# Kernel tuning notes

Measured on AMD Instinct MI355X. Metric: run time of the kernel, lower is better.

## Reference

```python
import jax, jax.numpy as jnp
import numpy as np

PS = 8          # patch_size
NF = 16         # n_feats
B, H, W = 4, 256, 256
C = NF * PS * PS          # channel_num = 1024
INNER = 3 * C             # heads * channel_num (no head split in source)
SCALE = C ** -0.5         # heads_feats = channel_num
EPS = 1e-5


def _patch(x, shift):
    # reflect-pad then non-overlapping unfold (kernel=PS, stride=PS)
    s = PS // 4
    p = shift * s
    x = jnp.pad(x, ((0, 0), (0, 0), (p, PS - p), (p, PS - p)), mode='reflect')
    b, c, hp, wp = x.shape
    x = x.reshape(b, c, hp // PS, PS, wp // PS, PS)
    # F.unfold ordering: (c, kh, kw) flattened per patch, patches row-major
    x = x.transpose(0, 2, 4, 1, 3, 5).reshape(b, (hp // PS) * (wp // PS), c * PS * PS)
    return x  # [B, N, C*PS*PS]


def _unpatch(x, h, w):
    # inverse of non-overlapping unfold, then crop right/bottom by PS
    b, n, d = x.shape
    c = d // (PS * PS)
    nh, nw = (h + PS) // PS, (w + PS) // PS
    x = x.reshape(b, nh, nw, c, PS, PS).transpose(0, 3, 1, 4, 2, 5)
    x = x.reshape(b, c, nh * PS, nw * PS)
    return x[:, :, :h, :w]


def _ln(x, g, b):
    m = x.mean(-1, keepdims=True)
    v = ((x - m) ** 2).mean(-1, keepdims=True)
    return (x - m) / jnp.sqrt(v + EPS) * g + b


def setup_inputs():
    key = jax.random.key(0)
    ks = jax.random.split(key, 16)
    w = lambda k, shp: jax.random.normal(k, shp, jnp.float32) * 0.02
    return {
        'dr_img': jax.random.normal(ks[0], (B, NF, H, W), jnp.float32),
        'dr_ref': jax.random.normal(ks[1], (B, NF, H, W), jnp.float32),
        'cl_ref': jax.random.normal(ks[2], (B, NF, H, W), jnp.float32),
        'ln_g': jnp.ones((C,), jnp.float32), 'ln_b': jnp.zeros((C,), jnp.float32),
        'Wq': w(ks[3], (C, INNER)), 'bq': jnp.zeros((INNER,), jnp.float32),
        'Wk': w(ks[4], (C, INNER)), 'bk': jnp.zeros((INNER,), jnp.float32),
        'Wv': w(ks[5], (C, INNER)), 'bv': jnp.zeros((INNER,), jnp.float32),
        'Wo': w(ks[6], (INNER, C)), 'bo': jnp.zeros((C,), jnp.float32),
        'ff_ln_g': jnp.ones((C,), jnp.float32), 'ff_ln_b': jnp.zeros((C,), jnp.float32),
        'W1': w(ks[7], (C, C)), 'b1': jnp.zeros((C,), jnp.float32),
        'W2': w(ks[8], (C, C)), 'b2': jnp.zeros((C,), jnp.float32),
    }


def reference(dr_img, dr_ref, cl_ref, ln_g, ln_b, Wq, bq, Wk, bk, Wv, bv,
              Wo, bo, ff_ln_g, ff_ln_b, W1, b1, W2, b2):
    def attn(q, k, v):
        qp = _ln(q, ln_g, ln_b) @ Wq + bq          # [B,N,3C]
        kp = _ln(k, ln_g, ln_b) @ Wk + bk
        vp = _ln(v, ln_g, ln_b) @ Wv + bv
        a = jax.nn.softmax(jnp.einsum('bnd,bmd->bnm', qp, kp) * SCALE, axis=-1)
        return jnp.einsum('bnm,bmd->bnd', a, vp) @ Wo + bo

    def ff(x):
        h = _ln(x, ff_ln_g, ff_ln_b)
        return jax.nn.gelu(h @ W1 + b1, approximate=False) @ W2 + b2

    x = _patch(dr_img, 0)                           # [B,N,C]
    for shift in range(4):
        k = jax.lax.stop_gradient(_patch(dr_ref, shift))
        v = jax.lax.stop_gradient(_patch(cl_ref, shift))
        x = attn(x, k, v) + x
        x = ff(x) + x
    return _unpatch(x, H, W)
```

## Files before the change

kernel.cpp:

```cpp
#include <hip/hip_runtime.h>

typedef unsigned short u16;
typedef float f32x4 __attribute__((ext_vector_type(4)));
typedef __bf16 bf16v8 __attribute__((ext_vector_type(8)));
typedef u16 u16x4 __attribute__((ext_vector_type(4)));

#define WAITV(n) asm volatile("s_waitcnt vmcnt(" #n ")" ::: "memory")
#define BAR() asm volatile("s_barrier" ::: "memory")
#define LGKM0() do { asm volatile("s_waitcnt lgkmcnt(0)" ::: "memory"); \
                     __builtin_amdgcn_sched_barrier(0); } while (0)

__device__ __forceinline__ u16 f2bf(float f) {
  union { float f; unsigned int u; } v; v.f = f;
  unsigned int x = v.u;
  x += 0x7fffu + ((x >> 16) & 1u);
  return (u16)(x >> 16);
}

__device__ __forceinline__ int refl(int i, int n) {
  i = (i < 0) ? -i : i;
  return (i >= n) ? (2 * n - 2 - i) : i;
}

__device__ __forceinline__ void gload_lds16(const void* g, void* l) {
  __builtin_amdgcn_global_load_lds(
      (const __attribute__((address_space(1))) void*)g,
      (__attribute__((address_space(3))) void*)l, 16, 0, 0);
}

enum { EPI_BF16_BIAS = 0, EPI_F32 = 1, EPI_BF16 = 2, EPI_F32_RES = 3, EPI_GELU = 4 };

__device__ __forceinline__ void xcd_remap(int& bx, int& by, int& bz) {
  const int gx = gridDim.x, gy = gridDim.y;
  const int nwg = gx * gy * (int)gridDim.z;
  const int orig = ((int)blockIdx.z * gy + (int)blockIdx.y) * gx + (int)blockIdx.x;
  const int q = nwg >> 3, r = nwg & 7;
  const int xcd = orig & 7, loc = orig >> 3;
  const int swz = (xcd < r ? xcd * (q + 1) : r * (q + 1) + (xcd - r) * q) + loc;
  const int gxy = gx * gy;
  bz = swz / gxy;
  const int rem = swz - bz * gxy;
  by = rem / gx; bx = rem - by * gx;
}

template <int EPI>
__global__ __launch_bounds__(512, 2) void gemm256(
    const u16* __restrict__ A, const u16* __restrict__ Bt, void* __restrict__ Cp,
    const float* __restrict__ bias, int K, int Nld, long sA, long sB, long sC, long sBias)
{
  extern __shared__ __align__(16) u16 smem[];

  const int t = threadIdx.x;
  int bx, by, bz; xcd_remap(bx, by, bz);
  const int m0 = by * 256, n0 = bx * 256;

  const long Kb = (long)K * 2;
  const int sr8 = t >> 3;
  const int schunk = ((t & 7) ^ (sr8 & 7)) * 16;
  const char* Ag = (const char*)(A + (long)bz * sA + (long)m0 * K) + (long)sr8 * Kb + schunk;
  const char* Bg = (const char*)(Bt + (long)bz * sB + (long)n0 * K) + (long)sr8 * Kb + schunk;

  auto SA = [&](int d, int kt, int i0, int i1) {
    const long ko = (long)kt * 128;
    gload_lds16(Ag + (long)i0 * 64 * Kb + ko, &smem[d * 32768 + i0 * 4096 + t * 8]);
    gload_lds16(Ag + (long)i1 * 64 * Kb + ko, &smem[d * 32768 + i1 * 4096 + t * 8]);
  };
  auto SB = [&](int d, int kt, int i0, int i1) {
    const long ko = (long)kt * 128;
    gload_lds16(Bg + (long)i0 * 64 * Kb + ko, &smem[d * 32768 + 16384 + i0 * 4096 + t * 8]);
    gload_lds16(Bg + (long)i1 * 64 * Kb + ko, &smem[d * 32768 + 16384 + i1 * 4096 + t * 8]);
  };

  const int w = t >> 6, lane = t & 63;
  const int wm = (w >> 2) * 128, wn = (w & 3) * 64;
  const int lr = lane & 15, hi = lane >> 4;
  const int rc0 = ((0 * 4 + hi) ^ (lr & 7)) * 8;
  const int rc1 = ((1 * 4 + hi) ^ (lr & 7)) * 8;

  f32x4 acc[8][4];
  const f32x4 vzero = {0.f, 0.f, 0.f, 0.f};
#pragma unroll
  for (int i = 0; i < 8; i++)
#pragma unroll
    for (int j = 0; j < 4; j++) acc[i][j] = vzero;

  const int NT = K >> 6, NI = NT >> 1;

  SA(0, 0, 0, 1); SA(0, 0, 2, 3); SB(0, 0, 0, 1); SB(0, 0, 2, 3);
  SB(1, 1, 0, 2); SB(1, 1, 1, 3); SA(1, 1, 0, 2);
  WAITV(6);
  BAR();

  for (int i = 0; i < NI; i++) {
    const int t0 = 2 * i;
    const bool last = (i == NI - 1);
#pragma unroll
    for (int h = 0; h < 2; h++) {
      const u16* Ad = &smem[h * 32768];
      const u16* Bd = Ad + 16384;
      bf16v8 b8[4][2];
#pragma unroll
      for (int q = 0; q < 4; q++) {
        bf16v8 a8[2][2];
#pragma unroll
        for (int j = 0; j < 2; j++) {
          const int rbase = (wm + (2 * q + j) * 16 + lr) * 64;
          a8[j][0] = *(const bf16v8*)&Ad[rbase + rc0];
          a8[j][1] = *(const bf16v8*)&Ad[rbase + rc1];
        }
        if (q == 0) {
#pragma unroll
          for (int ni = 0; ni < 4; ni++) {
            const int rbase = (wn + ni * 16 + lr) * 64;
            b8[ni][0] = *(const bf16v8*)&Bd[rbase + rc0];
            b8[ni][1] = *(const bf16v8*)&Bd[rbase + rc1];
          }
        }
        if (h == 0) {
          if (q == 0)           SA(1, t0 + 1, 1, 3);
          else if (!last) {
            if (q == 1)         SB(0, t0 + 2, 0, 2);
            else if (q == 2)    SB(0, t0 + 2, 1, 3);
            else                SA(0, t0 + 2, 0, 2);
          }
        } else if (!last) {
          if (q == 0)           SA(0, t0 + 2, 1, 3);
          else if (q == 1)      SB(1, t0 + 3, 0, 2);
          else if (q == 2)      SB(1, t0 + 3, 1, 3);
          else                  SA(1, t0 + 3, 0, 2);
        }
        BAR();
        LGKM0();
        __builtin_amdgcn_s_setprio(1);
#pragma unroll
        for (int j = 0; j < 2; j++)
#pragma unroll
          for (int ni = 0; ni < 4; ni++) {
            acc[2 * q + j][ni] = __builtin_amdgcn_mfma_f32_16x16x32_bf16(a8[j][0], b8[ni][0], acc[2 * q + j][ni], 0, 0, 0);
            acc[2 * q + j][ni] = __builtin_amdgcn_mfma_f32_16x16x32_bf16(a8[j][1], b8[ni][1], acc[2 * q + j][ni], 0, 0, 0);
          }
        __builtin_amdgcn_s_setprio(0);
        if (h == 0 && q == 3) { if (last) { WAITV(0); } else { WAITV(6); } }
        if (h == 1 && q == 3 && !last) { WAITV(6); }
        BAR();
      }
    }
  }

#pragma unroll
  for (int mi = 0; mi < 8; mi++) {
    const int r0 = m0 + wm + mi * 16 + hi * 4;
#pragma unroll
    for (int ni = 0; ni < 4; ni++) {
      const int col = n0 + wn + ni * 16 + lr;
      float bvv = 0.f;
      if constexpr (EPI == EPI_BF16_BIAS) bvv = bias[bz * sBias + col];
#pragma unroll
      for (int j = 0; j < 4; j++) {
        const long idx = (long)(r0 + j) * Nld + col;
        const float val = acc[mi][ni][j] + bvv;
        if constexpr (EPI == EPI_BF16_BIAS || EPI == EPI_BF16) {
          ((u16*)Cp + (long)bz * sC)[idx] = f2bf(val);
        } else {
          ((float*)Cp + (long)bz * sC)[idx] = val;
        }
      }
    }
  }
}

template <int EPI>
__global__ __launch_bounds__(256, 2) void gemm128(
    const u16* __restrict__ A, const u16* __restrict__ Bt, void* __restrict__ Cp,
    const float* __restrict__ bias, int K, int Nld, long sA, long sB, long sC)
{
  extern __shared__ __align__(16) u16 smem[];
  u16* As = smem;
  u16* Bs = smem + 16384;

  const int t = threadIdx.x;
  int bx, by, bz; xcd_remap(bx, by, bz);
  const int m0 = by * 128, n0 = bx * 128;

  const long Kb = (long)K * 2;
  const int sc = ((t & 7) * 16) ^ (((t >> 3) & 7) << 4);
  const char* Ag = (const char*)(A + (long)bz * sA + (long)m0 * K) + (long)(t >> 3) * Kb + sc;
  const char* Bg = (const char*)(Bt + (long)bz * sB + (long)n0 * K) + (long)(t >> 3) * Kb + sc;

  auto STAGE = [&](int d, int kt) {
    const long ko = (long)kt * 128;
#pragma unroll
    for (int i = 0; i < 4; i++)
      gload_lds16(Ag + (long)i * 32 * Kb + ko, &As[d * 8192 + i * 2048 + t * 8]);
#pragma unroll
    for (int i = 0; i < 4; i++)
      gload_lds16(Bg + (long)i * 32 * Kb + ko, &Bs[d * 8192 + i * 2048 + t * 8]);
  };

  const int w = t >> 6, lane = t & 63;
  const int wm = (w >> 1) * 64, wn = (w & 1) * 64;
  const int lr = lane & 15, hi = lane >> 4;
  const int cx = (lr & 7) << 4;

  f32x4 acc[4][4];
  const f32x4 vzero = {0.f, 0.f, 0.f, 0.f};
#pragma unroll
  for (int i = 0; i < 4; i++)
#pragma unroll
    for (int j = 0; j < 4; j++) acc[i][j] = vzero;

  const int NT = K >> 6;
  STAGE(0, 0);
  STAGE(1, 1);

  for (int kt = 0; kt < NT; kt++) {
    const int d = kt & 1;
    if (kt + 1 < NT) { WAITV(8); } else { WAITV(0); }
    BAR();

    const u16* Ad = &As[d * 8192];
    const u16* Bd = &Bs[d * 8192];
#pragma unroll
    for (int ks = 0; ks < 2; ks++) {
      bf16v8 a8[4], b8[4];
      const int cb = ks * 64;
#pragma unroll
      for (int mi = 0; mi < 4; mi++)
        a8[mi] = *(const bf16v8*)&Ad[(wm + mi * 16 + lr) * 64 + (((cb + hi * 16) ^ cx) >> 1)];
#pragma unroll
      for (int ni = 0; ni < 4; ni++)
        b8[ni] = *(const bf16v8*)&Bd[(wn + ni * 16 + lr) * 64 + (((cb + hi * 16) ^ cx) >> 1)];
      __builtin_amdgcn_s_setprio(1);
#pragma unroll
      for (int mi = 0; mi < 4; mi++)
#pragma unroll
        for (int ni = 0; ni < 4; ni++)
          acc[mi][ni] = __builtin_amdgcn_mfma_f32_16x16x32_bf16(a8[mi], b8[ni], acc[mi][ni], 0, 0, 0);
      __builtin_amdgcn_s_setprio(0);
    }
    asm volatile("s_waitcnt lgkmcnt(0)\n\ts_barrier" ::: "memory");
    if (kt + 2 < NT) STAGE(d, kt + 2);
  }

#pragma unroll
  for (int mi = 0; mi < 4; mi++) {
    const int r0 = m0 + wm + mi * 16 + hi * 4;
#pragma unroll
    for (int ni = 0; ni < 4; ni++) {
      const int col = n0 + wn + ni * 16 + lr;
      float bvv = 0.f;
      if constexpr (EPI == EPI_F32_RES || EPI == EPI_GELU) bvv = bias[col];
#pragma unroll
      for (int j = 0; j < 4; j++) {
        const long idx = (long)(r0 + j) * Nld + col;
        const float val = acc[mi][ni][j] + bvv;
        if constexpr (EPI == EPI_F32) {
          ((float*)Cp + (long)bz * sC)[idx] = val;
        } else if constexpr (EPI == EPI_F32_RES) {
          ((float*)Cp)[idx] += val;
        } else if constexpr (EPI == EPI_GELU) {
          const float gv = 0.5f * val * (1.f + erff(val * 0.70710678118654752440f));
          ((u16*)Cp)[idx] = f2bf(gv);
        } else {
          ((u16*)Cp)[idx] = f2bf(val);
        }
      }
    }
  }
}

__global__ __launch_bounds__(256) void ln_kernel(const float* __restrict__ X,
    const float* __restrict__ g, const float* __restrict__ be, u16* __restrict__ Y)
{
  const long row = blockIdx.x;
  const int t = threadIdx.x;
  const float* xr = X + row * 1024;
  f32x4 v = *(const f32x4*)&xr[t * 4];
  float s = v[0] + v[1] + v[2] + v[3];
  float q = v[0]*v[0] + v[1]*v[1] + v[2]*v[2] + v[3]*v[3];
#pragma unroll
  for (int off = 32; off; off >>= 1) { s += __shfl_xor(s, off); q += __shfl_xor(q, off); }
  __shared__ float red[8];
  if ((t & 63) == 0) { red[t >> 6] = s; red[4 + (t >> 6)] = q; }
  __syncthreads();
  s = red[0] + red[1] + red[2] + red[3];
  q = red[4] + red[5] + red[6] + red[7];
  const float mean = s * (1.f / 1024.f);
  const float rstd = rsqrtf(q * (1.f / 1024.f) - mean * mean + 1e-5f);
  f32x4 gv = *(const f32x4*)&g[t * 4];
  f32x4 bv = *(const f32x4*)&be[t * 4];
  u16x4 o;
#pragma unroll
  for (int i = 0; i < 4; i++) o[i] = f2bf((v[i] - mean) * rstd * gv[i] + bv[i]);
  *(u16x4*)&Y[row * 1024 + t * 4] = o;
}

__global__ __launch_bounds__(256) void patch_kernel(const float* __restrict__ img,
    float* __restrict__ X, int shift)
{
  const int n = blockIdx.x, b = blockIdx.y, t = threadIdx.x;
  float* xr = X + ((long)b * 1280 + n) * 1024;
  if (n >= 1089) {
    const f32x4 z = {0.f, 0.f, 0.f, 0.f};
    *(f32x4*)&xr[t * 4] = z;
    return;
  }
  const int p = shift * 2;
  const int ph = n / 33, pw = n - ph * 33;
  const int d0 = t * 4;
  const int c = d0 >> 6, kh = (d0 >> 3) & 7, kw0 = d0 & 7;
  const int hh = refl(ph * 8 + kh - p, 256);
  const float* src = img + ((long)(b * 16 + c) * 256 + hh) * 256;
  f32x4 v;
#pragma unroll
  for (int i = 0; i < 4; i++) v[i] = src[refl(pw * 8 + kw0 + i - p, 256)];
  *(f32x4*)&xr[d0] = v;
}

__global__ __launch_bounds__(256) void patch_ln_kernel(const float* __restrict__ img,
    const float* __restrict__ g, const float* __restrict__ be, u16* __restrict__ Y, int shift)
{
  const int n = blockIdx.x, b = blockIdx.y, t = threadIdx.x;
  u16* yr = Y + ((long)b * 1280 + n) * 1024;
  if (n >= 1089) {
    const u16x4 z = {0, 0, 0, 0};
    *(u16x4*)&yr[t * 4] = z;
    return;
  }
  const int p = shift * 2;
  const int ph = n / 33, pw = n - ph * 33;
  const int d0 = t * 4;
  const int c = d0 >> 6, kh = (d0 >> 3) & 7, kw0 = d0 & 7;
  const int hh = refl(ph * 8 + kh - p, 256);
  const float* src = img + ((long)(b * 16 + c) * 256 + hh) * 256;
  float v[4];
#pragma unroll
  for (int i = 0; i < 4; i++) v[i] = src[refl(pw * 8 + kw0 + i - p, 256)];
  float s = v[0] + v[1] + v[2] + v[3];
  float q = v[0]*v[0] + v[1]*v[1] + v[2]*v[2] + v[3]*v[3];
#pragma unroll
  for (int off = 32; off; off >>= 1) { s += __shfl_xor(s, off); q += __shfl_xor(q, off); }
  __shared__ float red[8];
  if ((t & 63) == 0) { red[t >> 6] = s; red[4 + (t >> 6)] = q; }
  __syncthreads();
  s = red[0] + red[1] + red[2] + red[3];
  q = red[4] + red[5] + red[6] + red[7];
  const float mean = s * (1.f / 1024.f);
  const float rstd = rsqrtf(q * (1.f / 1024.f) - mean * mean + 1e-5f);
  u16x4 o;
#pragma unroll
  for (int i = 0; i < 4; i++) o[i] = f2bf((v[i] - mean) * rstd * g[d0 + i] + be[d0 + i]);
  *(u16x4*)&yr[d0] = o;
}

__global__ __launch_bounds__(256) void softmax_kernel(const float* __restrict__ L,
    u16* __restrict__ P)
{
  const int r = blockIdx.x, b = blockIdx.y, t = threadIdx.x;
  const float* Lr = L + ((long)b * 1280 + r) * 1280;
  u16* Pr = P + ((long)b * 1280 + r) * 1280;
  float v[5];
  float mx = -1e30f;
#pragma unroll
  for (int i = 0; i < 5; i++) {
    const int j = t + i * 256;
    v[i] = (j < 1089) ? Lr[j] * 0.03125f : -1e30f;
    mx = fmaxf(mx, v[i]);
  }
#pragma unroll
  for (int off = 32; off; off >>= 1) mx = fmaxf(mx, __shfl_xor(mx, off));
  __shared__ float sm[4];
  if ((t & 63) == 0) sm[t >> 6] = mx;
  __syncthreads();
  mx = fmaxf(fmaxf(sm[0], sm[1]), fmaxf(sm[2], sm[3]));
  float p[5];
  float s = 0.f;
#pragma unroll
  for (int i = 0; i < 5; i++) {
    const int j = t + i * 256;
    p[i] = (j < 1089) ? __expf(v[i] - mx) : 0.f;
    s += p[i];
  }
#pragma unroll
  for (int off = 32; off; off >>= 1) s += __shfl_xor(s, off);
  __shared__ float ss[4];
  if ((t & 63) == 0) ss[t >> 6] = s;
  __syncthreads();
  const float inv = 1.f / (ss[0] + ss[1] + ss[2] + ss[3]);
#pragma unroll
  for (int i = 0; i < 5; i++) Pr[t + i * 256] = f2bf(p[i] * inv);
}

__global__ __launch_bounds__(256) void vtrans_kernel(const u16* __restrict__ V,
    u16* __restrict__ Vt)
{
  __shared__ u16 tile[32][33];
  const int b = blockIdx.z;
  const int d0 = blockIdx.x * 32, m0 = blockIdx.y * 32;
  const int tx = threadIdx.x & 31, ty = threadIdx.x >> 5;
  const u16* Vb = V + (long)b * 1280 * 3072;
  u16* Vtb = Vt + (long)b * 3072 * 1280;
#pragma unroll
  for (int i = 0; i < 4; i++)
    tile[ty + 8 * i][tx] = Vb[(long)(m0 + ty + 8 * i) * 3072 + d0 + tx];
  __syncthreads();
#pragma unroll
  for (int i = 0; i < 4; i++)
    Vtb[(long)(d0 + ty + 8 * i) * 1280 + m0 + tx] = tile[tx][ty + 8 * i];
}

__global__ __launch_bounds__(256) void wtrans_kernel(const float* __restrict__ W,
    u16* __restrict__ Wt, int K, int N)
{
  __shared__ float tile[32][33];
  const int n0 = blockIdx.x * 32, k0 = blockIdx.y * 32;
  const int tx = threadIdx.x & 31, ty = threadIdx.x >> 5;
#pragma unroll
  for (int i = 0; i < 4; i++)
    tile[ty + 8 * i][tx] = W[(long)(k0 + ty + 8 * i) * N + n0 + tx];
  __syncthreads();
#pragma unroll
  for (int i = 0; i < 4; i++)
    Wt[(long)(n0 + ty + 8 * i) * K + k0 + tx] = f2bf(tile[tx][ty + 8 * i]);
}

__global__ __launch_bounds__(256) void catbias_kernel(const float* __restrict__ a,
    const float* __restrict__ b, const float* __restrict__ c, float* __restrict__ o)
{
  const int i = blockIdx.x * 256 + threadIdx.x;
  o[i] = a[i]; o[3072 + i] = b[i]; o[6144 + i] = c[i];
}

__global__ __launch_bounds__(256) void unpatch_kernel(const float* __restrict__ X,
    float* __restrict__ out)
{
  const int idx = blockIdx.x * 256 + threadIdx.x;
  const int w = (idx & 63) * 4;
  const int h = (idx >> 6) & 255;
  const int c = (idx >> 14) & 15;
  const int b = idx >> 18;
  const int ph = h >> 3, kh = h & 7, pw = w >> 3, kw = w & 7;
  const long row = (long)b * 1280 + ph * 33 + pw;
  const int d = c * 64 + kh * 8 + kw;
  const f32x4 v = *(const f32x4*)&X[row * 1024 + d];
  *(f32x4*)&out[((long)(b * 16 + c) * 256 + h) * 256 + w] = v;
}

extern "C" void kernel_launch(void* const* d_in, const int* in_sizes, int n_in,
                              void* d_out, int out_size, void* d_ws, size_t ws_size,
                              hipStream_t stream)
{
  (void)in_sizes; (void)n_in; (void)out_size; (void)ws_size;
  const float* dr_img = (const float*)d_in[0];
  const float* dr_ref = (const float*)d_in[1];
  const float* cl_ref = (const float*)d_in[2];
  const float* ln_g = (const float*)d_in[3];
  const float* ln_be = (const float*)d_in[4];
  const float* Wq = (const float*)d_in[5];
  const float* bq = (const float*)d_in[6];
  const float* Wk = (const float*)d_in[7];
  const float* bk = (const float*)d_in[8];
  const float* Wv = (const float*)d_in[9];
  const float* bv = (const float*)d_in[10];
  const float* Wo = (const float*)d_in[11];
  const float* bo = (const float*)d_in[12];
  const float* ffg = (const float*)d_in[13];
  const float* ffb = (const float*)d_in[14];
  const float* W1 = (const float*)d_in[15];
  const float* b1 = (const float*)d_in[16];
  const float* W2 = (const float*)d_in[17];
  const float* b2 = (const float*)d_in[18];

  const long R = 1280;
  const long MR = 4 * R;

  char* ws = (char*)d_ws;
  size_t off = 0;
  auto alloc = [&](size_t bytes) -> void* {
    void* pp = ws + off;
    off += (bytes + 255) & ~(size_t)255;
    return pp;
  };
  float* x    = (float*)alloc((size_t)MR * 1024 * 4);
  u16* xkv_ln = (u16*)alloc((size_t)3 * MR * 1024 * 2);
  u16* qkv    = (u16*)alloc((size_t)3 * MR * 3072 * 2);
  float* lgt  = (float*)alloc((size_t)4 * R * R * 4);
  u16* P      = (u16*)alloc((size_t)4 * R * R * 2);
  u16* Wqkv_t = (u16*)alloc((size_t)3 * 3072 * 1024 * 2);
  u16* Wo_t   = (u16*)alloc((size_t)1024 * 3072 * 2);
  u16* W1_t   = (u16*)alloc((size_t)1024 * 1024 * 2);
  u16* W2_t   = (u16*)alloc((size_t)1024 * 1024 * 2);
  float* bcat = (float*)alloc((size_t)3 * 3072 * 4);

  u16* x_ln = xkv_ln;
  u16* h    = xkv_ln + (size_t)MR * 1024;
  u16* qp   = qkv;
  u16* kp   = qkv + (size_t)MR * 3072;
  u16* vp   = qkv + (size_t)2 * MR * 3072;

  wtrans_kernel<<<dim3(96, 32), 256, 0, stream>>>(Wq, Wqkv_t, 1024, 3072);
  wtrans_kernel<<<dim3(96, 32), 256, 0, stream>>>(Wk, Wqkv_t + (size_t)3072 * 1024, 1024, 3072);
  wtrans_kernel<<<dim3(96, 32), 256, 0, stream>>>(Wv, Wqkv_t + (size_t)2 * 3072 * 1024, 1024, 3072);
  wtrans_kernel<<<dim3(32, 96), 256, 0, stream>>>(Wo, Wo_t, 3072, 1024);
  wtrans_kernel<<<dim3(32, 32), 256, 0, stream>>>(W1, W1_t, 1024, 1024);
  wtrans_kernel<<<dim3(32, 32), 256, 0, stream>>>(W2, W2_t, 1024, 1024);
  catbias_kernel<<<12, 256, 0, stream>>>(bq, bk, bv, bcat);

  patch_kernel<<<dim3(1280, 4), 256, 0, stream>>>(dr_img, x, 0);

  const long sAp = (long)MR * 1024;
  const long sBp = (long)3072 * 1024;
  const long sCp = (long)MR * 3072;
  const long sQb = R * 3072;
  const long sLb = R * R;

  for (int shift = 0; shift < 4; shift++) {
    ln_kernel<<<(int)MR, 256, 0, stream>>>(x, ln_g, ln_be, x_ln);
    patch_ln_kernel<<<dim3(1280, 4), 256, 0, stream>>>(dr_ref, ln_g, ln_be, xkv_ln + sAp, shift);
    patch_ln_kernel<<<dim3(1280, 4), 256, 0, stream>>>(cl_ref, ln_g, ln_be, xkv_ln + 2 * sAp, shift);

    gemm256<EPI_BF16_BIAS><<<dim3(12, 20, 3), 512, 131072, stream>>>(
        xkv_ln, Wqkv_t, qkv, bcat, 1024, 3072, sAp, sBp, sCp, 3072);

    gemm128<EPI_F32><<<dim3(10, 10, 4), 256, 65536, stream>>>(
        qp, kp, lgt, nullptr, 3072, 1280, sQb, sQb, sLb);

    softmax_kernel<<<dim3(1280, 4), 256, 0, stream>>>(lgt, P);
    vtrans_kernel<<<dim3(96, 40, 4), 256, 0, stream>>>(vp, kp);

    gemm256<EPI_BF16><<<dim3(12, 5, 4), 512, 131072, stream>>>(
        P, kp, qp, nullptr, 1280, 3072, sLb, (long)3072 * R, sQb, 0);

    gemm128<EPI_F32_RES><<<dim3(8, 40, 1), 256, 65536, stream>>>(
        qp, Wo_t, x, bo, 3072, 1024, 0, 0, 0);

    ln_kernel<<<(int)MR, 256, 0, stream>>>(x, ffg, ffb, x_ln);
    gemm128<EPI_GELU><<<dim3(8, 40, 1), 256, 65536, stream>>>(
        x_ln, W1_t, h, b1, 1024, 1024, 0, 0, 0);
    gemm128<EPI_F32_RES><<<dim3(8, 40, 1), 256, 65536, stream>>>(
        h, W2_t, x, b2, 1024, 1024, 0, 0, 0);
  }

  unpatch_kernel<<<4096, 256, 0, stream>>>(x, (float*)d_out);
}
```

Baseline: 1.486 ms.

## Shrink per-batch padding to 1152 rows and compute V projection pre-transposed

Per-batch patch rows are now padded to 1152 instead of 1280, which trims wasted rows from every GEMM, softmax and LN launch; the attention GEMMs, which scale quadratically with row count, shrink the most. The V projection becomes its own GEMM computing Wv^T·LN(v)^T with a per-row bias epilogue, so V comes out already transposed. That removes the separate vtrans kernel. The PV product moves to the 128-tile GEMM, which gains a separate B leading dimension and batch stride on its outputs. The risks are correctness of the padded-key handling at the new size and a worse tile fit for the split V GEMM.

After: 1.408 ms. 5.3% less time.

```diff
diff --git a/kernel.cpp b/kernel.cpp
--- a/kernel.cpp
+++ b/kernel.cpp
@@ -28,7 +28,8 @@
       (__attribute__((address_space(3))) void*)l, 16, 0, 0);
 }
 
-enum { EPI_BF16_BIAS = 0, EPI_F32 = 1, EPI_BF16 = 2, EPI_F32_RES = 3, EPI_GELU = 4 };
+enum { EPI_BF16_BIAS = 0, EPI_F32 = 1, EPI_BF16 = 2, EPI_F32_RES = 3, EPI_GELU = 4,
+       EPI_BF16_BIASROW = 5 };
 
 __device__ __forceinline__ void xcd_remap(int& bx, int& by, int& bz) {
   const int gx = gridDim.x, gy = gridDim.y;
@@ -158,8 +159,9 @@
 #pragma unroll
       for (int j = 0; j < 4; j++) {
         const long idx = (long)(r0 + j) * Nld + col;
-        const float val = acc[mi][ni][j] + bvv;
-        if constexpr (EPI == EPI_BF16_BIAS || EPI == EPI_BF16) {
+        float val = acc[mi][ni][j] + bvv;
+        if constexpr (EPI == EPI_BF16_BIASROW) val += bias[r0 + j];
+        if constexpr (EPI == EPI_BF16_BIAS || EPI == EPI_BF16 || EPI == EPI_BF16_BIASROW) {
           ((u16*)Cp + (long)bz * sC)[idx] = f2bf(val);
         } else {
           ((float*)Cp + (long)bz * sC)[idx] = val;
@@ -172,7 +174,7 @@
 template <int EPI>
 __global__ __launch_bounds__(256, 2) void gemm128(
     const u16* __restrict__ A, const u16* __restrict__ Bt, void* __restrict__ Cp,
-    const float* __restrict__ bias, int K, int Nld, long sA, long sB, long sC)
+    const float* __restrict__ bias, int K, int ldb, int Nld, long sA, long sB, long sC)
 {
   extern __shared__ __align__(16) u16 smem[];
   u16* As = smem;
@@ -182,19 +184,20 @@
   int bx, by, bz; xcd_remap(bx, by, bz);
   const int m0 = by * 128, n0 = bx * 128;
 
-  const long Kb = (long)K * 2;
+  const long Ka = (long)K * 2;
+  const long Kbb = (long)ldb * 2;
   const int sc = ((t & 7) * 16) ^ (((t >> 3) & 7) << 4);
-  const char* Ag = (const char*)(A + (long)bz * sA + (long)m0 * K) + (long)(t >> 3) * Kb + sc;
-  const char* Bg = (const char*)(Bt + (long)bz * sB + (long)n0 * K) + (long)(t >> 3) * Kb + sc;
+  const char* Ag = (const char*)(A + (long)bz * sA + (long)m0 * K) + (long)(t >> 3) * Ka + sc;
+  const char* Bg = (const char*)(Bt + (long)bz * sB + (long)n0 * ldb) + (long)(t >> 3) * Kbb + sc;
 
   auto STAGE = [&](int d, int kt) {
     const long ko = (long)kt * 128;
 #pragma unroll
     for (int i = 0; i < 4; i++)
-      gload_lds16(Ag + (long)i * 32 * Kb + ko, &As[d * 8192 + i * 2048 + t * 8]);
+      gload_lds16(Ag + (long)i * 32 * Ka + ko, &As[d * 8192 + i * 2048 + t * 8]);
 #pragma unroll
     for (int i = 0; i < 4; i++)
-      gload_lds16(Bg + (long)i * 32 * Kb + ko, &Bs[d * 8192 + i * 2048 + t * 8]);
+      gload_lds16(Bg + (long)i * 32 * Kbb + ko, &Bs[d * 8192 + i * 2048 + t * 8]);
   };
 
   const int w = t >> 6, lane = t & 63;
@@ -257,12 +260,12 @@
         if constexpr (EPI == EPI_F32) {
           ((float*)Cp + (long)bz * sC)[idx] = val;
         } else if constexpr (EPI == EPI_F32_RES) {
-          ((float*)Cp)[idx] += val;
+          ((float*)Cp + (long)bz * sC)[idx] += val;
         } else if constexpr (EPI == EPI_GELU) {
           const float gv = 0.5f * val * (1.f + erff(val * 0.70710678118654752440f));
-          ((u16*)Cp)[idx] = f2bf(gv);
+          ((u16*)Cp + (long)bz * sC)[idx] = f2bf(gv);
         } else {
-          ((u16*)Cp)[idx] = f2bf(val);
+          ((u16*)Cp + (long)bz * sC)[idx] = f2bf(val);
         }
       }
     }
@@ -299,7 +302,7 @@
     float* __restrict__ X, int shift)
 {
   const int n = blockIdx.x, b = blockIdx.y, t = threadIdx.x;
-  float* xr = X + ((long)b * 1280 + n) * 1024;
+  float* xr = X + ((long)b * 1152 + n) * 1024;
   if (n >= 1089) {
     const f32x4 z = {0.f, 0.f, 0.f, 0.f};
     *(f32x4*)&xr[t * 4] = z;
@@ -321,7 +324,7 @@
     const float* __restrict__ g, const float* __restrict__ be, u16* __restrict__ Y, int shift)
 {
   const int n = blockIdx.x, b = blockIdx.y, t = threadIdx.x;
-  u16* yr = Y + ((long)b * 1280 + n) * 1024;
+  u16* yr = Y + ((long)b * 1152 + n) * 1024;
   if (n >= 1089) {
     const u16x4 z = {0, 0, 0, 0};
     *(u16x4*)&yr[t * 4] = z;
@@ -357,8 +360,8 @@
     u16* __restrict__ P)
 {
   const int r = blockIdx.x, b = blockIdx.y, t = threadIdx.x;
-  const float* Lr = L + ((long)b * 1280 + r) * 1280;
-  u16* Pr = P + ((long)b * 1280 + r) * 1280;
+  const float* Lr = L + ((long)b * 1152 + r) * 1152;
+  u16* Pr = P + ((long)b * 1152 + r) * 1152;
   float v[5];
   float mx = -1e30f;
 #pragma unroll
@@ -388,25 +391,10 @@
   __syncthreads();
   const float inv = 1.f / (ss[0] + ss[1] + ss[2] + ss[3]);
 #pragma unroll
-  for (int i = 0; i < 5; i++) Pr[t + i * 256] = f2bf(p[i] * inv);
-}
-
-__global__ __launch_bounds__(256) void vtrans_kernel(const u16* __restrict__ V,
-    u16* __restrict__ Vt)
-{
-  __shared__ u16 tile[32][33];
-  const int b = blockIdx.z;
-  const int d0 = blockIdx.x * 32, m0 = blockIdx.y * 32;
-  const int tx = threadIdx.x & 31, ty = threadIdx.x >> 5;
-  const u16* Vb = V + (long)b * 1280 * 3072;
-  u16* Vtb = Vt + (long)b * 3072 * 1280;
-#pragma unroll
-  for (int i = 0; i < 4; i++)
-    tile[ty + 8 * i][tx] = Vb[(long)(m0 + ty + 8 * i) * 3072 + d0 + tx];
-  __syncthreads();
-#pragma unroll
-  for (int i = 0; i < 4; i++)
-    Vtb[(long)(d0 + ty + 8 * i) * 1280 + m0 + tx] = tile[tx][ty + 8 * i];
+  for (int i = 0; i < 5; i++) {
+    const int j = t + i * 256;
+    if (j < 1152) Pr[j] = f2bf(p[i] * inv);
+  }
 }
 
 __global__ __launch_bounds__(256) void wtrans_kernel(const float* __restrict__ W,
@@ -440,7 +428,7 @@
   const int c = (idx >> 14) & 15;
   const int b = idx >> 18;
   const int ph = h >> 3, kh = h & 7, pw = w >> 3, kw = w & 7;
-  const long row = (long)b * 1280 + ph * 33 + pw;
+  const long row = (long)b * 1152 + ph * 33 + pw;
   const int d = c * 64 + kh * 8 + kw;
   const f32x4 v = *(const f32x4*)&X[row * 1024 + d];
   *(f32x4*)&out[((long)(b * 16 + c) * 256 + h) * 256 + w] = v;
@@ -471,7 +459,7 @@
   const float* W2 = (const float*)d_in[17];
   const float* b2 = (const float*)d_in[18];
 
-  const long R = 1280;
+  const long R = 1152;
   const long MR = 4 * R;
 
   char* ws = (char*)d_ws;
@@ -493,20 +481,22 @@
   float* bcat = (float*)alloc((size_t)3 * 3072 * 4);
 
   u16* x_ln = xkv_ln;
+  u16* v_ln = xkv_ln + (size_t)2 * MR * 1024;
   u16* h    = xkv_ln + (size_t)MR * 1024;
   u16* qp   = qkv;
   u16* kp   = qkv + (size_t)MR * 3072;
-  u16* vp   = qkv + (size_t)2 * MR * 3072;
+  u16* vT   = qkv + (size_t)2 * MR * 3072;
+  u16* Wv_t = Wqkv_t + (size_t)2 * 3072 * 1024;
 
   wtrans_kernel<<<dim3(96, 32), 256, 0, stream>>>(Wq, Wqkv_t, 1024, 3072);
   wtrans_kernel<<<dim3(96, 32), 256, 0, stream>>>(Wk, Wqkv_t + (size_t)3072 * 1024, 1024, 3072);
-  wtrans_kernel<<<dim3(96, 32), 256, 0, stream>>>(Wv, Wqkv_t + (size_t)2 * 3072 * 1024, 1024, 3072);
+  wtrans_kernel<<<dim3(96, 32), 256, 0, stream>>>(Wv, Wv_t, 1024, 3072);
   wtrans_kernel<<<dim3(32, 96), 256, 0, stream>>>(Wo, Wo_t, 3072, 1024);
   wtrans_kernel<<<dim3(32, 32), 256, 0, stream>>>(W1, W1_t, 1024, 1024);
   wtrans_kernel<<<dim3(32, 32), 256, 0, stream>>>(W2, W2_t, 1024, 1024);
   catbias_kernel<<<12, 256, 0, stream>>>(bq, bk, bv, bcat);
 
-  patch_kernel<<<dim3(1280, 4), 256, 0, stream>>>(dr_img, x, 0);
+  patch_kernel<<<dim3(1152, 4), 256, 0, stream>>>(dr_img, x, 0);
 
   const long sAp = (long)MR * 1024;
   const long sBp = (long)3072 * 1024;
@@ -516,29 +506,31 @@
 
   for (int shift = 0; shift < 4; shift++) {
     ln_kernel<<<(int)MR, 256, 0, stream>>>(x, ln_g, ln_be, x_ln);
-    patch_ln_kernel<<<dim3(1280, 4), 256, 0, stream>>>(dr_ref, ln_g, ln_be, xkv_ln + sAp, shift);
-    patch_ln_kernel<<<dim3(1280, 4), 256, 0, stream>>>(cl_ref, ln_g, ln_be, xkv_ln + 2 * sAp, shift);
-
-    gemm256<EPI_BF16_BIAS><<<dim3(12, 20, 3), 512, 131072, stream>>>(
+    patch_ln_kernel<<<dim3(1152, 4), 256, 0, stream>>>(dr_ref, ln_g, ln_be, xkv_ln + sAp, shift);
+    patch_ln_kernel<<<dim3(1152, 4), 256, 0, stream>>>(cl_ref, ln_g, ln_be, v_ln, shift);
+
+    gemm256<EPI_BF16_BIAS><<<dim3(12, 18, 2), 512, 131072, stream>>>(
         xkv_ln, Wqkv_t, qkv, bcat, 1024, 3072, sAp, sBp, sCp, 3072);
 
-    gemm128<EPI_F32><<<dim3(10, 10, 4), 256, 65536, stream>>>(
-        qp, kp, lgt, nullptr, 3072, 1280, sQb, sQb, sLb);
-
-    softmax_kernel<<<dim3(1280, 4), 256, 0, stream>>>(lgt, P);
-    vtrans_kernel<<<dim3(96, 40, 4), 256, 0, stream>>>(vp, kp);
-
-    gemm256<EPI_BF16><<<dim3(12, 5, 4), 512, 131072, stream>>>(
-        P, kp, qp, nullptr, 1280, 3072, sLb, (long)3072 * R, sQb, 0);
-
-    gemm128<EPI_F32_RES><<<dim3(8, 40, 1), 256, 65536, stream>>>(
-        qp, Wo_t, x, bo, 3072, 1024, 0, 0, 0);
+    gemm256<EPI_BF16_BIASROW><<<dim3(18, 12, 1), 512, 131072, stream>>>(
+        Wv_t, v_ln, vT, bv, 1024, (int)MR, 0, 0, 0, 0);
+
+    gemm128<EPI_F32><<<dim3(9, 9, 4), 256, 65536, stream>>>(
+        qp, kp, lgt, nullptr, 3072, 3072, 1152, sQb, sQb, sLb);
+
+    softmax_kernel<<<dim3(1152, 4), 256, 0, stream>>>(lgt, P);
+
+    gemm128<EPI_BF16><<<dim3(24, 9, 4), 256, 65536, stream>>>(
+        P, vT, qp, nullptr, 1152, (int)MR, 3072, sLb, R, sQb);
+
+    gemm128<EPI_F32_RES><<<dim3(8, 36, 1), 256, 65536, stream>>>(
+        qp, Wo_t, x, bo, 3072, 3072, 1024, 0, 0, 0);
 
     ln_kernel<<<(int)MR, 256, 0, stream>>>(x, ffg, ffb, x_ln);
-    gemm128<EPI_GELU><<<dim3(8, 40, 1), 256, 65536, stream>>>(
-        x_ln, W1_t, h, b1, 1024, 1024, 0, 0, 0);
-    gemm128<EPI_F32_RES><<<dim3(8, 40, 1), 256, 65536, stream>>>(
-        h, W2_t, x, b2, 1024, 1024, 0, 0, 0);
+    gemm128<EPI_GELU><<<dim3(8, 36, 1), 256, 65536, stream>>>(
+        x_ln, W1_t, h, b1, 1024, 1024, 1024, 0, 0, 0);
+    gemm128<EPI_F32_RES><<<dim3(8, 36, 1), 256, 65536, stream>>>(
+        h, W2_t, x, b2, 1024, 1024, 1024, 0, 0, 0);
   }
 
   unpatch_kernel<<<4096, 256, 0, stream>>>(x, (float*)d_out);
```
